# Kernel optimization log

Measured on AMD Instinct MI355X. Metric: run time of the kernel, lower is better.

The kernel has to match this reference:

```python
import jax, jax.numpy as jnp
import numpy as np

N_SRC = 50000
N_DST1 = 20000
N_DST2 = 10000
E1 = 320000
E2 = 160000
T = 12
C_IN = 64
HID = 16
C_OUT = 32


def _gat_layer(src_feat, dst_feat, src_idx, dst_idx, ew, W, a_l, a_r, n_dst):
    # src_feat: [N_src, T, C], dst_feat: [N_dst, T, C]
    h_src = jnp.einsum('ntc,co->nto', src_feat, W)   # [N_src, T, O]
    h_dst = jnp.einsum('ntc,co->nto', dst_feat, W)   # [N_dst, T, O]
    el = jnp.einsum('nto,o->nt', h_src, a_l)          # [N_src, T]
    er = jnp.einsum('nto,o->nt', h_dst, a_r)          # [N_dst, T]
    # per-edge attention logits
    e = jax.nn.leaky_relu(el[src_idx] + er[dst_idx], negative_slope=0.2)  # [E, T]
    # segment softmax over incoming edges of each dst node
    m = jax.ops.segment_max(e, dst_idx, num_segments=n_dst)               # [N_dst, T]
    ex = jnp.exp(e - m[dst_idx])
    s = jax.ops.segment_sum(ex, dst_idx, num_segments=n_dst)
    alpha = ex / (s[dst_idx] + 1e-9)                                      # [E, T]
    msg = (alpha * ew[:, None])[:, :, None] * h_src[src_idx]              # [E, T, O]
    return jax.ops.segment_sum(msg, dst_idx, num_segments=n_dst)          # [N_dst, T, O]


def setup_inputs() -> dict:
    key = jax.random.key(0)
    ks = jax.random.split(key, 12)
    inp = {
        'node_feat': jax.random.normal(ks[0], (T, N_SRC, C_IN), dtype=jnp.float32),
        'edge_src1': jax.random.randint(ks[1], (E1,), 0, N_SRC, dtype=jnp.int32),
        'edge_dst1': jax.random.randint(ks[2], (E1,), 0, N_DST1, dtype=jnp.int32),
        'edge_weight1': jax.random.uniform(ks[3], (E1,), dtype=jnp.float32),
        'edge_src2': jax.random.randint(ks[4], (E2,), 0, N_DST1, dtype=jnp.int32),
        'edge_dst2': jax.random.randint(ks[5], (E2,), 0, N_DST2, dtype=jnp.int32),
        'edge_weight2': jax.random.uniform(ks[6], (E2,), dtype=jnp.float32),
        'W1': jax.random.normal(ks[7], (C_IN, HID), dtype=jnp.float32) * (1.0 / np.sqrt(C_IN)),
        'a_l1': jax.random.normal(ks[8], (HID,), dtype=jnp.float32) * 0.1,
        'a_r1': jax.random.normal(ks[9], (HID,), dtype=jnp.float32) * 0.1,
        'W2': jax.random.normal(ks[10], (HID, C_OUT), dtype=jnp.float32) * (1.0 / np.sqrt(HID)),
        'a_l2': jax.random.normal(ks[11], (C_OUT,), dtype=jnp.float32) * 0.1,
        'a_r2': jax.random.normal(jax.random.fold_in(key, 99), (C_OUT,), dtype=jnp.float32) * 0.1,
    }
    return inp


def reference(node_feat, edge_src1, edge_dst1, edge_weight1,
              edge_src2, edge_dst2, edge_weight2,
              W1, a_l1, a_r1, W2, a_l2, a_r2):
    # [T, N, C] -> [N, T, C]
    x = jnp.transpose(node_feat, (1, 0, 2))
    h1 = _gat_layer(x, x[:N_DST1], edge_src1, edge_dst1, edge_weight1,
                    W1, a_l1, a_r1, N_DST1)
    h1 = jax.nn.leaky_relu(h1, negative_slope=0.01)
    h2 = _gat_layer(h1, h1[:N_DST2], edge_src2, edge_dst2, edge_weight2,
                    W2, a_l2, a_r2, N_DST2)
    h2 = jax.nn.leaky_relu(h2, negative_slope=0.01)
    # [N_dst2, T, O] -> [T, N_dst2, O]
    return jnp.transpose(h2, (1, 0, 2))
```

## Files before the change

kernel.cpp:

```cpp
#include <hip/hip_runtime.h>

#define N_SRC 50000
#define N_DST1 20000
#define N_DST2 10000
#define E1 320000
#define E2 160000
#define T 12
#define C_IN 64
#define HID 16
#define C_OUT 32
#define EB 1875
#define TB 782

__device__ __forceinline__ float lrelu(float x, float s) { return x > 0.f ? x : s * x; }

__device__ __forceinline__ int xcd_swizzle(int p, int W) {
    int x = p & 7, k = p >> 3;
    int q = W >> 3, r = W & 7;
    return (x < r ? x * (q + 1) : r * (q + 1) + (x - r) * q) + k;
}

__global__ __launch_bounds__(256) void k_zero(int4* __restrict__ p, int n4)
{
    int i = blockIdx.x * 256 + threadIdx.x;
    if (i < n4) p[i] = make_int4(0, 0, 0, 0);
}

__device__ __forceinline__ void transform_tile(
    int nblk, int t, int tx,
    const float* __restrict__ nf, const float* __restrict__ W1,
    const float* __restrict__ a_l, const float* __restrict__ a_r,
    float* __restrict__ hs1, float* __restrict__ el1, float* __restrict__ er1)
{
    __shared__ float xs[64][68];
    __shared__ float w[C_IN][HID];
    __shared__ float al[HID], ar[HID];
    int n0 = nblk * 64;
    int nrem = N_SRC - n0; if (nrem > 64) nrem = 64;

    reinterpret_cast<float4*>(&w[0][0])[tx] = reinterpret_cast<const float4*>(W1)[tx];
    if (tx < HID) al[tx] = a_l[tx];
    else if (tx < 2 * HID) ar[tx - HID] = a_r[tx - HID];

    const float4* gp = reinterpret_cast<const float4*>(nf + ((size_t)t * N_SRC + n0) * C_IN);
#pragma unroll
    for (int k = 0; k < 4; k++) {
        int f = k * 256 + tx;
        int node = f >> 4;
        if (node < nrem)
            *reinterpret_cast<float4*>(&xs[node][(f & 15) * 4]) = gp[f];
    }
    __syncthreads();

    int q = tx & 3;
    int nn = tx >> 2;
    float4 acc = make_float4(0.f, 0.f, 0.f, 0.f);
#pragma unroll
    for (int c4 = 0; c4 < 16; c4++) {
        float4 xA = *reinterpret_cast<const float4*>(&xs[nn][c4 * 4]);
        float4 w0 = *reinterpret_cast<const float4*>(&w[c4 * 4 + 0][q * 4]);
        float4 w1 = *reinterpret_cast<const float4*>(&w[c4 * 4 + 1][q * 4]);
        float4 w2 = *reinterpret_cast<const float4*>(&w[c4 * 4 + 2][q * 4]);
        float4 w3 = *reinterpret_cast<const float4*>(&w[c4 * 4 + 3][q * 4]);
        acc.x += xA.x * w0.x + xA.y * w1.x + xA.z * w2.x + xA.w * w3.x;
        acc.y += xA.x * w0.y + xA.y * w1.y + xA.z * w2.y + xA.w * w3.y;
        acc.z += xA.x * w0.z + xA.y * w1.z + xA.z * w2.z + xA.w * w3.z;
        acc.w += xA.x * w0.w + xA.y * w1.w + xA.z * w2.w + xA.w * w3.w;
    }

    float el = acc.x * al[q * 4] + acc.y * al[q * 4 + 1] + acc.z * al[q * 4 + 2] + acc.w * al[q * 4 + 3];
    float er = acc.x * ar[q * 4] + acc.y * ar[q * 4 + 1] + acc.z * ar[q * 4 + 2] + acc.w * ar[q * 4 + 3];
    el += __shfl_xor(el, 1); el += __shfl_xor(el, 2);
    er += __shfl_xor(er, 1); er += __shfl_xor(er, 2);

    if (nn < nrem) {
        float* hb = hs1 + ((size_t)t * N_SRC + n0) * HID;
        *reinterpret_cast<float4*>(hb + (size_t)nn * HID + q * 4) = acc;
        if (q == 0) {
            int n = n0 + nn;
            el1[(size_t)t * N_SRC + n] = el;
            if (n < N_DST1) er1[(size_t)t * N_DST1 + n] = er;
        }
    }
}

__global__ __launch_bounds__(256) void k_A(
    const int* __restrict__ d1, const int* __restrict__ d2,
    int* __restrict__ cnt1, int* __restrict__ cnt2,
    const float* __restrict__ nf, const float* __restrict__ W1,
    const float* __restrict__ a_l, const float* __restrict__ a_r,
    float* __restrict__ hs1, float* __restrict__ el1, float* __restrict__ er1)
{
    if (blockIdx.x < EB) {
        int e = blockIdx.x * 256 + threadIdx.x;
        if (e < E1) atomicAdd(&cnt1[d1[e]], 1);
        else atomicAdd(&cnt2[d2[e - E1]], 1);
        return;
    }
    int idx = blockIdx.x - EB;
    transform_tile(idx % TB, idx / TB, threadIdx.x,
                   nf, W1, a_l, a_r, hs1, el1, er1);
}

__global__ __launch_bounds__(256) void k_B(
    const int* __restrict__ s1, const int* __restrict__ d1, const float* __restrict__ w1,
    int* __restrict__ cur1, int2* __restrict__ sw1,
    const int* __restrict__ s2, const int* __restrict__ d2, const float* __restrict__ w2,
    int* __restrict__ cur2, int2* __restrict__ sw2,
    const float* __restrict__ nf, const float* __restrict__ W1,
    const float* __restrict__ a_l, const float* __restrict__ a_r,
    float* __restrict__ hs1, float* __restrict__ el1, float* __restrict__ er1)
{
    if (blockIdx.x < EB) {
        int e = blockIdx.x * 256 + threadIdx.x;
        if (e < E1) {
            int d = d1[e];
            int p = atomicAdd(&cur1[d], 1);
            sw1[p] = make_int2(s1[e], __float_as_int(w1[e]));
        } else {
            int ee = e - E1;
            int d = d2[ee];
            int p = atomicAdd(&cur2[d], 1);
            sw2[p] = make_int2(s2[ee], __float_as_int(w2[ee]));
        }
        return;
    }
    int idx = blockIdx.x - EB;
    transform_tile(idx % TB, 6 + idx / TB, threadIdx.x,
                   nf, W1, a_l, a_r, hs1, el1, er1);
}

__device__ void scan_one(const int* cnt, int* off, int* cur, int N)
{
    __shared__ int part[1024];
    int tx = threadIdx.x;
    int CH = (N + 1023) / 1024;
    int base = tx * CH;
    int p = 0;
    for (int k = 0; k < CH; k++) { int i = base + k; if (i < N) p += cnt[i]; }
    part[tx] = p;
    __syncthreads();
#pragma unroll
    for (int d = 1; d < 1024; d <<= 1) {
        int v = (tx >= d) ? part[tx - d] : 0;
        __syncthreads();
        part[tx] += v;
        __syncthreads();
    }
    int run = (tx == 0) ? 0 : part[tx - 1];
    if (tx == 0) off[0] = 0;
    for (int k = 0; k < CH; k++) {
        int i = base + k;
        if (i < N) { cur[i] = run; run += cnt[i]; off[i + 1] = run; }
    }
}

__global__ __launch_bounds__(1024) void k_scan(
    const int* __restrict__ cnt1, int* __restrict__ off1, int* __restrict__ cur1,
    const int* __restrict__ cnt2, int* __restrict__ off2, int* __restrict__ cur2,
    const float* __restrict__ W2, const float* __restrict__ al2,
    const float* __restrict__ ar2, float* __restrict__ wl2, float* __restrict__ wr2)
{
    if (blockIdx.x == 2) {
        int tx = threadIdx.x;
        if (tx < 32) {
            int c = tx & 15;
            const float* a = (tx < 16) ? al2 : ar2;
            float s = 0.f;
            for (int o = 0; o < C_OUT; o++) s += W2[c * C_OUT + o] * a[o];
            if (tx < 16) wl2[c] = s; else wr2[c] = s;
        }
        return;
    }
    if (blockIdx.x == 0) scan_one(cnt1, off1, cur1, N_DST1);
    else                 scan_one(cnt2, off2, cur2, N_DST2);
}

#define EDGE1(I)                                                                \
    {                                                                           \
        int2 sa = sw[I];                                                        \
        float ea = elb[sa.x];                                                   \
        float4 ha = *reinterpret_cast<const float4*>(hsb + (size_t)sa.x * HID + q * 4); \
        float exa = __expf(lrelu(ea + erv, 0.2f));                              \
        den += exa;                                                             \
        float ca = exa * __int_as_float(sa.y);                                  \
        num.x += ca * ha.x; num.y += ca * ha.y;                                 \
        num.z += ca * ha.z; num.w += ca * ha.w;                                 \
    }

template <int NDST, int NSRC, bool FINAL>
__global__ __launch_bounds__(256) void k_gat(
    const int* __restrict__ off, const int2* __restrict__ sw,
    const float* __restrict__ el, const float* __restrict__ er,
    const float* __restrict__ hs, float* __restrict__ outp,
    const float* __restrict__ wl, const float* __restrict__ wr,
    float* __restrict__ el_out, float* __restrict__ er_out)
{
    __shared__ float w2s[FINAL ? HID * C_OUT : 1];
    int tx = threadIdx.x;
    if (FINAL) {
        for (int idx = tx; idx < HID * C_OUT; idx += 256) w2s[idx] = wl[idx];
        __syncthreads();
    }
    int wblk = xcd_swizzle(blockIdx.x, (NDST * T) / 16);
    int grp = tx >> 4;
    int lane16 = tx & 15;
    int q = lane16 & 3;
    int eslot = lane16 >> 2;
    int g = wblk * 16 + grp;
    int t = g / NDST;
    int d = g - t * NDST;
    int start = off[d], end = off[d + 1];
    float erv = er[g];
    const float* elb = el + (size_t)t * NSRC;
    const float* hsb = hs + (size_t)t * NSRC * HID;

    float4 num = make_float4(0.f, 0.f, 0.f, 0.f);
    float den = 0.f;
    int i = start + eslot;
    for (; i + 12 < end; i += 16) {
        int2 sa = sw[i];
        int2 sb = sw[i + 4];
        int2 sc = sw[i + 8];
        int2 sd = sw[i + 12];
        float ea = elb[sa.x];
        float eb = elb[sb.x];
        float ec = elb[sc.x];
        float ed = elb[sd.x];
        float4 ha = *reinterpret_cast<const float4*>(hsb + (size_t)sa.x * HID + q * 4);
        float4 hb = *reinterpret_cast<const float4*>(hsb + (size_t)sb.x * HID + q * 4);
        float4 hc = *reinterpret_cast<const float4*>(hsb + (size_t)sc.x * HID + q * 4);
        float4 hd = *reinterpret_cast<const float4*>(hsb + (size_t)sd.x * HID + q * 4);
        float exa = __expf(lrelu(ea + erv, 0.2f));
        float exb = __expf(lrelu(eb + erv, 0.2f));
        float exc = __expf(lrelu(ec + erv, 0.2f));
        float exd = __expf(lrelu(ed + erv, 0.2f));
        den += (exa + exb) + (exc + exd);
        float ca = exa * __int_as_float(sa.y);
        float cb = exb * __int_as_float(sb.y);
        float cc = exc * __int_as_float(sc.y);
        float cd = exd * __int_as_float(sd.y);
        num.x += ca * ha.x + cb * hb.x + cc * hc.x + cd * hd.x;
        num.y += ca * ha.y + cb * hb.y + cc * hc.y + cd * hd.y;
        num.z += ca * ha.z + cb * hb.z + cc * hc.z + cd * hd.z;
        num.w += ca * ha.w + cb * hb.w + cc * hc.w + cd * hd.w;
    }
    for (; i + 4 < end; i += 8) {
        int2 sa = sw[i];
        int2 sb = sw[i + 4];
        float ea = elb[sa.x];
        float eb = elb[sb.x];
        float4 ha = *reinterpret_cast<const float4*>(hsb + (size_t)sa.x * HID + q * 4);
        float4 hb = *reinterpret_cast<const float4*>(hsb + (size_t)sb.x * HID + q * 4);
        float exa = __expf(lrelu(ea + erv, 0.2f));
        float exb = __expf(lrelu(eb + erv, 0.2f));
        den += exa + exb;
        float ca = exa * __int_as_float(sa.y);
        float cb = exb * __int_as_float(sb.y);
        num.x += ca * ha.x + cb * hb.x;
        num.y += ca * ha.y + cb * hb.y;
        num.z += ca * ha.z + cb * hb.z;
        num.w += ca * ha.w + cb * hb.w;
    }
    if (i < end) EDGE1(i);
#pragma unroll
    for (int mk = 4; mk <= 8; mk <<= 1) {
        num.x += __shfl_xor(num.x, mk);
        num.y += __shfl_xor(num.y, mk);
        num.z += __shfl_xor(num.z, mk);
        num.w += __shfl_xor(num.w, mk);
        den   += __shfl_xor(den, mk);
    }
    float inv = 1.f / (den + 1e-9f);
    float4 v = make_float4(num.x * inv, num.y * inv, num.z * inv, num.w * inv);

    if (!FINAL) {
        v.x = lrelu(v.x, 0.01f); v.y = lrelu(v.y, 0.01f);
        v.z = lrelu(v.z, 0.01f); v.w = lrelu(v.w, 0.01f);
        if (eslot == 0) {
            *reinterpret_cast<float4*>(outp + (size_t)g * HID + q * 4) = v;
            float pl = v.x * wl[q * 4] + v.y * wl[q * 4 + 1] + v.z * wl[q * 4 + 2] + v.w * wl[q * 4 + 3];
            float pr = v.x * wr[q * 4] + v.y * wr[q * 4 + 1] + v.z * wr[q * 4 + 2] + v.w * wr[q * 4 + 3];
            pl += __shfl_xor(pl, 1); pl += __shfl_xor(pl, 2);
            pr += __shfl_xor(pr, 1); pr += __shfl_xor(pr, 2);
            if (q == 0) {
                el_out[g] = pl;
                if (d < N_DST2) er_out[(size_t)t * N_DST2 + d] = pr;
            }
        }
    } else {
        float4 v1, v2, v3;
        v1.x = __shfl_xor(v.x, 1); v1.y = __shfl_xor(v.y, 1); v1.z = __shfl_xor(v.z, 1); v1.w = __shfl_xor(v.w, 1);
        v2.x = __shfl_xor(v.x, 2); v2.y = __shfl_xor(v.y, 2); v2.z = __shfl_xor(v.z, 2); v2.w = __shfl_xor(v.w, 2);
        v3.x = __shfl_xor(v.x, 3); v3.y = __shfl_xor(v.y, 3); v3.z = __shfl_xor(v.z, 3); v3.w = __shfl_xor(v.w, 3);
        int obase = q * 8;
        float out8[8];
#pragma unroll
        for (int oo = 0; oo < 8; oo++) out8[oo] = 0.f;
#define ACCQ(Q, R0)                                                             \
        {                                                                       \
            int r0 = (R0) * 4;                                                  \
            _Pragma("unroll")                                                   \
            for (int oo = 0; oo < 8; oo++)                                      \
                out8[oo] += (Q).x * w2s[(r0 + 0) * C_OUT + obase + oo]          \
                          + (Q).y * w2s[(r0 + 1) * C_OUT + obase + oo]          \
                          + (Q).z * w2s[(r0 + 2) * C_OUT + obase + oo]          \
                          + (Q).w * w2s[(r0 + 3) * C_OUT + obase + oo];         \
        }
        ACCQ(v,  q);
        ACCQ(v1, q ^ 1);
        ACCQ(v2, q ^ 2);
        ACCQ(v3, q ^ 3);
#undef ACCQ
        if (eslot == 0) {
            float* op = outp + (size_t)g * C_OUT + obase;
            float4 w0 = make_float4(lrelu(out8[0], 0.01f), lrelu(out8[1], 0.01f),
                                    lrelu(out8[2], 0.01f), lrelu(out8[3], 0.01f));
            float4 w1 = make_float4(lrelu(out8[4], 0.01f), lrelu(out8[5], 0.01f),
                                    lrelu(out8[6], 0.01f), lrelu(out8[7], 0.01f));
            *reinterpret_cast<float4*>(op) = w0;
            *reinterpret_cast<float4*>(op + 4) = w1;
        }
    }
}

extern "C" void kernel_launch(void* const* d_in, const int* in_sizes, int n_in,
                              void* d_out, int out_size, void* d_ws, size_t ws_size,
                              hipStream_t stream)
{
    const float* node_feat = (const float*)d_in[0];
    const int*   esrc1     = (const int*)d_in[1];
    const int*   edst1     = (const int*)d_in[2];
    const float* ew1       = (const float*)d_in[3];
    const int*   esrc2     = (const int*)d_in[4];
    const int*   edst2     = (const int*)d_in[5];
    const float* ew2       = (const float*)d_in[6];
    const float* W1        = (const float*)d_in[7];
    const float* a_l1      = (const float*)d_in[8];
    const float* a_r1      = (const float*)d_in[9];
    const float* W2        = (const float*)d_in[10];
    const float* a_l2      = (const float*)d_in[11];
    const float* a_r2      = (const float*)d_in[12];
    float* out = (float*)d_out;

    float* ws = (float*)d_ws;
    float* hs1 = ws;
    float* el1 = hs1 + 9600000;
    float* er1 = el1 + 600000;
    float* h1  = er1 + 240000;
    float* el2 = h1 + 3840000;
    float* er2 = el2 + 240000;
    float* wl2 = er2 + 120000;
    float* wr2 = wl2 + 16;
    int2* sw1 = (int2*)(wr2 + 16);
    int2* sw2 = sw1 + E1;
    int* cnt1 = (int*)(sw2 + E2);
    int* cnt2 = cnt1 + N_DST1;
    int* off1 = cnt2 + N_DST2;
    int* cur1 = off1 + N_DST1 + 1;
    int* off2 = cur1 + N_DST1;
    int* cur2 = off2 + N_DST2 + 1;

    k_zero<<<30, 256, 0, stream>>>((int4*)cnt1, (N_DST1 + N_DST2) / 4);
    k_A<<<EB + TB * 6, 256, 0, stream>>>(edst1, edst2, cnt1, cnt2,
                                         node_feat, W1, a_l1, a_r1, hs1, el1, er1);
    k_scan<<<3, 1024, 0, stream>>>(cnt1, off1, cur1, cnt2, off2, cur2,
                                   W2, a_l2, a_r2, wl2, wr2);
    k_B<<<EB + TB * 6, 256, 0, stream>>>(esrc1, edst1, ew1, cur1, sw1,
                                         esrc2, edst2, ew2, cur2, sw2,
                                         node_feat, W1, a_l1, a_r1, hs1, el1, er1);
    k_gat<N_DST1, N_SRC, false><<<(N_DST1 * T) / 16, 256, 0, stream>>>(
        off1, sw1, el1, er1, hs1, h1, wl2, wr2, el2, er2);
    k_gat<N_DST2, N_DST1, true><<<(N_DST2 * T) / 16, 256, 0, stream>>>(
        off2, sw2, el2, er2, h1, out, W2, nullptr, nullptr, nullptr);
}
```

Baseline: 211.6 us.

## Replace global-atomic degree counting with per-block LDS histograms and restructure pre-kernels

Degree counting now runs in 15 blocks that each own a 2000-node range of destinations, build a shared-memory histogram and write counts directly. This removes the separate zero kernel and the contended global atomics. All 12 feature-transform timesteps now run in one kernel next to the histogram blocks, and edge scatter becomes its own kernel instead of overlapping with half the transform. Each histogram block scans the whole edge list (320k or 160k edges), so those few blocks may become a long tail, and the scatter no longer overlaps with transform work.

```diff
diff --git a/kernel.cpp b/kernel.cpp
--- a/kernel.cpp
+++ b/kernel.cpp
@@ -9,8 +9,8 @@
 #define C_IN 64
 #define HID 16
 #define C_OUT 32
-#define EB 1875
 #define TB 782
+#define HB 15
 
 __device__ __forceinline__ float lrelu(float x, float s) { return x > 0.f ? x : s * x; }
 
@@ -20,14 +20,9 @@
     return (x < r ? x * (q + 1) : r * (q + 1) + (x - r) * q) + k;
 }
 
-__global__ __launch_bounds__(256) void k_zero(int4* __restrict__ p, int n4)
-{
-    int i = blockIdx.x * 256 + threadIdx.x;
-    if (i < n4) p[i] = make_int4(0, 0, 0, 0);
-}
-
-__device__ __forceinline__ void transform_tile(
-    int nblk, int t, int tx,
+__global__ __launch_bounds__(256) void k_pre(
+    const int* __restrict__ d1, const int* __restrict__ d2,
+    int* __restrict__ cnt1, int* __restrict__ cnt2,
     const float* __restrict__ nf, const float* __restrict__ W1,
     const float* __restrict__ a_l, const float* __restrict__ a_r,
     float* __restrict__ hs1, float* __restrict__ el1, float* __restrict__ er1)
@@ -35,6 +30,28 @@
     __shared__ float xs[64][68];
     __shared__ float w[C_IN][HID];
     __shared__ float al[HID], ar[HID];
+    int tx = threadIdx.x;
+
+    if (blockIdx.x < HB) {
+        int* hist = (int*)&xs[0][0];
+        int b = blockIdx.x;
+        const int* dsrc; int E, lo; int* cnt;
+        if (b < 10) { dsrc = d1; E = E1; lo = b * 2000; cnt = cnt1; }
+        else        { dsrc = d2; E = E2; lo = (b - 10) * 2000; cnt = cnt2; }
+        for (int i = tx; i < 2000; i += 256) hist[i] = 0;
+        __syncthreads();
+        for (int e = tx; e < E; e += 256) {
+            int d = dsrc[e] - lo;
+            if ((unsigned)d < 2000u) atomicAdd(&hist[d], 1);
+        }
+        __syncthreads();
+        for (int i = tx; i < 2000; i += 256) cnt[lo + i] = hist[i];
+        return;
+    }
+
+    int idx = blockIdx.x - HB;
+    int nblk = idx % TB;
+    int t = idx / TB;
     int n0 = nblk * 64;
     int nrem = N_SRC - n0; if (nrem > 64) nrem = 64;
 
@@ -84,52 +101,6 @@
     }
 }
 
-__global__ __launch_bounds__(256) void k_A(
-    const int* __restrict__ d1, const int* __restrict__ d2,
-    int* __restrict__ cnt1, int* __restrict__ cnt2,
-    const float* __restrict__ nf, const float* __restrict__ W1,
-    const float* __restrict__ a_l, const float* __restrict__ a_r,
-    float* __restrict__ hs1, float* __restrict__ el1, float* __restrict__ er1)
-{
-    if (blockIdx.x < EB) {
-        int e = blockIdx.x * 256 + threadIdx.x;
-        if (e < E1) atomicAdd(&cnt1[d1[e]], 1);
-        else atomicAdd(&cnt2[d2[e - E1]], 1);
-        return;
-    }
-    int idx = blockIdx.x - EB;
-    transform_tile(idx % TB, idx / TB, threadIdx.x,
-                   nf, W1, a_l, a_r, hs1, el1, er1);
-}
-
-__global__ __launch_bounds__(256) void k_B(
-    const int* __restrict__ s1, const int* __restrict__ d1, const float* __restrict__ w1,
-    int* __restrict__ cur1, int2* __restrict__ sw1,
-    const int* __restrict__ s2, const int* __restrict__ d2, const float* __restrict__ w2,
-    int* __restrict__ cur2, int2* __restrict__ sw2,
-    const float* __restrict__ nf, const float* __restrict__ W1,
-    const float* __restrict__ a_l, const float* __restrict__ a_r,
-    float* __restrict__ hs1, float* __restrict__ el1, float* __restrict__ er1)
-{
-    if (blockIdx.x < EB) {
-        int e = blockIdx.x * 256 + threadIdx.x;
-        if (e < E1) {
-            int d = d1[e];
-            int p = atomicAdd(&cur1[d], 1);
-            sw1[p] = make_int2(s1[e], __float_as_int(w1[e]));
-        } else {
-            int ee = e - E1;
-            int d = d2[ee];
-            int p = atomicAdd(&cur2[d], 1);
-            sw2[p] = make_int2(s2[ee], __float_as_int(w2[ee]));
-        }
-        return;
-    }
-    int idx = blockIdx.x - EB;
-    transform_tile(idx % TB, 6 + idx / TB, threadIdx.x,
-                   nf, W1, a_l, a_r, hs1, el1, er1);
-}
-
 __device__ void scan_one(const int* cnt, int* off, int* cur, int N)
 {
     __shared__ int part[1024];
@@ -174,6 +145,25 @@
     }
     if (blockIdx.x == 0) scan_one(cnt1, off1, cur1, N_DST1);
     else                 scan_one(cnt2, off2, cur2, N_DST2);
+}
+
+__global__ __launch_bounds__(256) void k_scatter(
+    const int* __restrict__ s1, const int* __restrict__ d1, const float* __restrict__ w1,
+    int* __restrict__ cur1, int2* __restrict__ sw1,
+    const int* __restrict__ s2, const int* __restrict__ d2, const float* __restrict__ w2,
+    int* __restrict__ cur2, int2* __restrict__ sw2)
+{
+    int e = blockIdx.x * 256 + threadIdx.x;
+    if (e < E1) {
+        int d = d1[e];
+        int p = atomicAdd(&cur1[d], 1);
+        sw1[p] = make_int2(s1[e], __float_as_int(w1[e]));
+    } else if (e < E1 + E2) {
+        int ee = e - E1;
+        int d = d2[ee];
+        int p = atomicAdd(&cur2[d], 1);
+        sw2[p] = make_int2(s2[ee], __float_as_int(w2[ee]));
+    }
 }
 
 #define EDGE1(I)                                                                \
@@ -361,14 +351,13 @@
     int* off2 = cur1 + N_DST1;
     int* cur2 = off2 + N_DST2 + 1;
 
-    k_zero<<<30, 256, 0, stream>>>((int4*)cnt1, (N_DST1 + N_DST2) / 4);
-    k_A<<<EB + TB * 6, 256, 0, stream>>>(edst1, edst2, cnt1, cnt2,
-                                         node_feat, W1, a_l1, a_r1, hs1, el1, er1);
+    k_pre<<<HB + TB * T, 256, 0, stream>>>(edst1, edst2, cnt1, cnt2,
+                                           node_feat, W1, a_l1, a_r1, hs1, el1, er1);
     k_scan<<<3, 1024, 0, stream>>>(cnt1, off1, cur1, cnt2, off2, cur2,
                                    W2, a_l2, a_r2, wl2, wr2);
-    k_B<<<EB + TB * 6, 256, 0, stream>>>(esrc1, edst1, ew1, cur1, sw1,
-                                         esrc2, edst2, ew2, cur2, sw2,
-                                         node_feat, W1, a_l1, a_r1, hs1, el1, er1);
+    k_scatter<<<(E1 + E2 + 255) / 256, 256, 0, stream>>>(
+        esrc1, edst1, ew1, cur1, sw1,
+        esrc2, edst2, ew2, cur2, sw2);
     k_gat<N_DST1, N_SRC, false><<<(N_DST1 * T) / 16, 256, 0, stream>>>(
         off1, sw1, el1, er1, hs1, h1, wl2, wr2, el2, er2);
     k_gat<N_DST2, N_DST1, true><<<(N_DST2 * T) / 16, 256, 0, stream>>>(
```

After: 530.5 us. +150.7%, slower.
